# Kernel optimization log

Measured on AMD Instinct MI355X. Metric: run time of the kernel, lower is better.

Reference implementation:

```python
import jax, jax.numpy as jnp
import numpy as np

V = 100000   # vocab_size
E = 300      # embedding_dim
H = 512      # hidden_dim
HH = H // 2  # per-direction hidden
T = 24       # tagset size (incl START/STOP)
START, STOP = 22, 23
S = 4096     # sentence length
NEG = -10000.0


def setup_inputs() -> dict:
    key = jax.random.key(0)
    ks = jax.random.split(key, 12)
    sc = 0.05
    trans = jax.random.normal(ks[10], (T, T), jnp.float32) * 0.01
    # no transition INTO START, none OUT OF STOP (tutorial convention: trans[to, from])
    trans = trans.at[START, :].set(NEG).at[:, STOP].set(NEG)
    return {
        "sentence": jax.random.randint(ks[0], (S,), 0, V),
        "emb_table": jax.random.normal(ks[1], (V, E), jnp.float32) * sc,
        "w_ih_f": jax.random.normal(ks[2], (4 * HH, E), jnp.float32) * sc,
        "w_hh_f": jax.random.normal(ks[3], (4 * HH, HH), jnp.float32) * sc,
        "b_f": jnp.zeros((4 * HH,), jnp.float32),
        "w_ih_b": jax.random.normal(ks[4], (4 * HH, E), jnp.float32) * sc,
        "w_hh_b": jax.random.normal(ks[5], (4 * HH, HH), jnp.float32) * sc,
        "b_b": jnp.zeros((4 * HH,), jnp.float32),
        "w_tag": jax.random.normal(ks[6], (T, H), jnp.float32) * sc,
        "b_tag": jnp.zeros((T,), jnp.float32),
        "transitions": trans,
    }


def _lstm(x, w_ih, w_hh, b, reverse):
    # PyTorch LSTM gate order: i, f, g, o
    def step(carry, xt):
        h, c = carry
        g = xt @ w_ih.T + h @ w_hh.T + b
        i, f, gg, o = jnp.split(g, 4)
        c = jax.nn.sigmoid(f) * c + jax.nn.sigmoid(i) * jnp.tanh(gg)
        h = jax.nn.sigmoid(o) * jnp.tanh(c)
        return (h, c), h
    init = (jnp.zeros((HH,), x.dtype), jnp.zeros((HH,), x.dtype))
    _, hs = jax.lax.scan(step, init, x, reverse=reverse)
    return hs  # [S, HH], in original time order for both directions


def reference(sentence, emb_table, w_ih_f, w_hh_f, b_f, w_ih_b, w_hh_b, b_b,
              w_tag, b_tag, transitions):
    x = emb_table[sentence]                                   # [S, E]
    h = jnp.concatenate([_lstm(x, w_ih_f, w_hh_f, b_f, False),
                         _lstm(x, w_ih_b, w_hh_b, b_b, True)], axis=-1)  # [S, H]
    feats = h @ w_tag.T + b_tag                               # [S, T] emissions

    # Viterbi decode (tutorial _viterbi_decode)
    vinit = jnp.full((T,), NEG, feats.dtype).at[START].set(0.0)

    def vstep(v, feat):
        scores = v[None, :] + transitions                     # [to, from]
        return jnp.max(scores, axis=1) + feat, jnp.argmax(scores, axis=1)

    v, bptrs = jax.lax.scan(vstep, vinit, feats)              # bptrs: [S, T]
    term = v + transitions[STOP]
    best = jnp.argmax(term)
    score = term[best]

    def back(tag, bp):
        return bp[tag], tag

    _, path = jax.lax.scan(back, best, bptrs, reverse=True)   # [S] best tag seq
    return score, path
```

## Files before the change

kernel.cpp:

```cpp
#include <hip/hip_runtime.h>
#include <hip/hip_bf16.h>

#define S_LEN 4096
#define NTAG 24
#define START_TAG 22
#define STOP_TAG 23
#define SENT 0x7F800001u

static const size_t OFF_WT    = 0;
static const size_t OFF_XG    = OFF_WT + (size_t)300*2048*4;
static const size_t OFF_HS    = OFF_XG + (size_t)2*4096*1024*4;
static const size_t OFF_FEATS = OFF_HS + (size_t)2*4096*256*4;
static const size_t OFF_BP    = OFF_FEATS + (size_t)4096*24*4;
static const size_t OFF_WALK  = OFF_XG;

__device__ __forceinline__ float sigf(float x) {
    return __fdividef(1.f, 1.f + __expf(-x));
}
__device__ __forceinline__ float tanhfast(float x) {
    return 1.f - __fdividef(2.f, 1.f + __expf(2.f * x));
}

__device__ __forceinline__ float4 load_f4_sc1(const float* p) {
    float4 v;
    asm volatile("global_load_dwordx4 %0, %1, off sc1\n\t"
                 "s_waitcnt vmcnt(0)"
                 : "=v"(v) : "v"(p) : "memory");
    return v;
}

__device__ __forceinline__ float atomic_poll_word(const float* p) {
    float v;
    do {
        v = __hip_atomic_load(p, __ATOMIC_RELAXED, __HIP_MEMORY_SCOPE_AGENT);
    } while (__float_as_uint(v) == SENT);
    return v;
}

__global__ void prep_kernel(const float* __restrict__ w_ih_f, const float* __restrict__ w_ih_b,
                            float* __restrict__ WT, unsigned int* __restrict__ HSu) {
    int tid = blockIdx.x * blockDim.x + threadIdx.x;
    int nth = gridDim.x * blockDim.x;
    for (int idx = tid; idx < 300 * 2048; idx += nth) {
        int k = idx / 2048, col = idx % 2048;
        WT[idx] = (col < 1024) ? w_ih_f[col * 300 + k] : w_ih_b[(col - 1024) * 300 + k];
    }
    for (int idx = tid; idx < 2 * S_LEN * 256; idx += nth)
        HSu[idx] = SENT;
}

__global__ __launch_bounds__(256) void embed_xg_kernel(const int* __restrict__ sentence,
                                                       const float* __restrict__ emb,
                                                       const float* __restrict__ WT,
                                                       const float* __restrict__ b_f,
                                                       const float* __restrict__ b_b,
                                                       float* __restrict__ xg) {
    __shared__ float xs[16][300];
    int s0 = blockIdx.x * 16;
    for (int idx = threadIdx.x; idx < 16 * 300; idx += 256) {
        int si = idx / 300, k = idx - si * 300;
        int wrow = sentence[s0 + si];
        xs[si][k] = emb[(size_t)wrow * 300 + k];
    }
    __syncthreads();
    for (int chunk = 0; chunk < 8; ++chunk) {
        int col = chunk * 256 + threadIdx.x;
        float acc[16];
#pragma unroll
        for (int s = 0; s < 16; ++s) acc[s] = 0.f;
        for (int k = 0; k < 300; k += 4) {
            float w0 = WT[(k + 0) * 2048 + col];
            float w1 = WT[(k + 1) * 2048 + col];
            float w2 = WT[(k + 2) * 2048 + col];
            float w3 = WT[(k + 3) * 2048 + col];
#pragma unroll
            for (int s = 0; s < 16; ++s) {
                float4 x4 = *reinterpret_cast<const float4*>(&xs[s][k]);
                acc[s] += w0 * x4.x + w1 * x4.y + w2 * x4.z + w3 * x4.w;
            }
        }
        int dir = col >> 10;
        int row = col & 1023;
        float bias = dir ? b_b[row] : b_f[row];
#pragma unroll
        for (int s = 0; s < 16; ++s)
            xg[((size_t)dir * S_LEN + (s0 + s)) * 1024 + row] = acc[s] + bias;
    }
}

__global__ __launch_bounds__(1024) void lstm_kernel(const float* __restrict__ xg,
                                                    const float* __restrict__ w_hh_f,
                                                    const float* __restrict__ w_hh_b,
                                                    float* __restrict__ hs) {
    const int xslot = blockIdx.x & 7;
    if (xslot > 1) return;
    const int dir = xslot;
    const int blk = blockIdx.x >> 3;
    const int tid = threadIdx.x;
    const int r4 = tid >> 5;
    const int kc = tid & 31;

    __shared__ float hsk[32 * 10];
    __shared__ float part[128][33];
    __shared__ float gl[128];

    const float* whh = dir ? w_hh_b : w_hh_f;
    float w[4][8];
#pragma unroll
    for (int q = 0; q < 4; ++q) {
        int R = r4 * 4 + q;
        int grow = ((R >> 5) << 8) + blk * 32 + (R & 31);
#pragma unroll
        for (int j = 0; j < 8; ++j)
            w[q][j] = whh[(size_t)grow * 256 + kc * 8 + j];
    }

    for (int i = tid; i < 320; i += 1024) hsk[i] = 0.f;

    const float* xgd = xg + (size_t)dir * S_LEN * 1024;
    float* hsd = hs + (size_t)dir * S_LEN * 256;
    float c = 0.f;
    int growR = 0;
    float xg_cur = 0.f;
    if (tid < 128) {
        growR = ((tid >> 5) << 8) + blk * 32 + (tid & 31);
        xg_cur = xgd[(size_t)(dir ? (S_LEN - 1) : 0) * 1024 + growR];
    }
    __syncthreads();

    for (int step = 0; step < S_LEN; ++step) {
        const int st = dir ? (S_LEN - 1 - step) : step;

        float hv[8];
        const int hb = kc * 10;
#pragma unroll
        for (int j = 0; j < 8; ++j) hv[j] = hsk[hb + j];
        float p0 = 0.f, p1 = 0.f, p2 = 0.f, p3 = 0.f;
#pragma unroll
        for (int j = 0; j < 8; ++j) {
            p0 += w[0][j] * hv[j];
            p1 += w[1][j] * hv[j];
            p2 += w[2][j] * hv[j];
            p3 += w[3][j] * hv[j];
        }
        part[r4 * 4 + 0][kc] = p0;
        part[r4 * 4 + 1][kc] = p1;
        part[r4 * 4 + 2][kc] = p2;
        part[r4 * 4 + 3][kc] = p3;
        __syncthreads();

        float xg_nxt = 0.f;
        if (tid < 128) {
            if (step + 1 < S_LEN) {
                const int stn = dir ? (st - 1) : (st + 1);
                xg_nxt = xgd[(size_t)stn * 1024 + growR];
            }
            float a0 = 0.f, a1 = 0.f, a2 = 0.f, a3 = 0.f;
#pragma unroll
            for (int k2 = 0; k2 < 32; k2 += 4) {
                a0 += part[tid][k2 + 0];
                a1 += part[tid][k2 + 1];
                a2 += part[tid][k2 + 2];
                a3 += part[tid][k2 + 3];
            }
            gl[tid] = xg_cur + ((a0 + a1) + (a2 + a3));
        }
        __syncthreads();

        if (tid < 32) {
            float gi = gl[tid], gf = gl[32 + tid], gg = gl[64 + tid], go = gl[96 + tid];
            float si = sigf(gi), sf = sigf(gf), so = sigf(go);
            c = sf * c + si * tanhfast(gg);
            float h = so * tanhfast(c);
            __hip_atomic_store(&hsd[(size_t)st * 256 + blk * 32 + tid], h,
                               __ATOMIC_RELAXED, __HIP_MEMORY_SCOPE_AGENT);
            int w0 = blk * 32 + tid;
            hsk[(w0 >> 3) * 10 + (w0 & 7)] = h;
        }
        else if (tid >= 128 && tid < 192 && step + 1 < S_LEN) {
            const int l = tid - 128;
            if ((l >> 3) != blk) {
                const float* src = &hsd[(size_t)st * 256 + l * 4];
                float4 v;
                int spins = 0;
                bool ok;
                do {
                    v = load_f4_sc1(src);
                    ok = !(__float_as_uint(v.x) == SENT || __float_as_uint(v.y) == SENT ||
                           __float_as_uint(v.z) == SENT || __float_as_uint(v.w) == SENT);
                } while (!ok && ++spins < 512);
                if (!ok) {
                    v.x = atomic_poll_word(src + 0);
                    v.y = atomic_poll_word(src + 1);
                    v.z = atomic_poll_word(src + 2);
                    v.w = atomic_poll_word(src + 3);
                }
                const int w0 = l * 4;
                const int base = (w0 >> 3) * 10 + (w0 & 7);
                hsk[base + 0] = v.x;
                hsk[base + 1] = v.y;
                hsk[base + 2] = v.z;
                hsk[base + 3] = v.w;
            }
        }
        xg_cur = xg_nxt;
        __syncthreads();
    }
}

__global__ __launch_bounds__(384) void feats_kernel(const float* __restrict__ hs,
                                                    const float* __restrict__ w_tag,
                                                    const float* __restrict__ b_tag,
                                                    float* __restrict__ feats) {
    __shared__ float ht[16][512];
    int s0 = blockIdx.x * 16;
    for (int idx = threadIdx.x; idx < 16 * 512; idx += 384) {
        int si = idx >> 9, k = idx & 511;
        float v = (k < 256) ? hs[(size_t)(s0 + si) * 256 + k]
                            : hs[(size_t)S_LEN * 256 + (size_t)(s0 + si) * 256 + (k - 256)];
        ht[si][k] = v;
    }
    __syncthreads();
    int si = threadIdx.x / NTAG;
    int t = threadIdx.x - si * NTAG;
    float acc = b_tag[t];
    const float* wr = w_tag + t * 512;
    for (int k = 0; k < 512; k += 4) {
        float4 w4 = *reinterpret_cast<const float4*>(&wr[k]);
        float4 h4 = *reinterpret_cast<const float4*>(&ht[si][k]);
        acc += w4.x * h4.x + w4.y * h4.y + w4.z * h4.z + w4.w * h4.w;
    }
    feats[(size_t)(s0 + si) * NTAG + t] = acc;
}

__global__ __launch_bounds__(1024) void viterbi_kernel(const float* __restrict__ feats,
                                                       const float* __restrict__ trans,
                                                       unsigned char* __restrict__ bp_g,
                                                       unsigned char* __restrict__ walk_g,
                                                       float* __restrict__ out) {
    const int tid = threadIdx.x;
    __shared__ float s_bv;
    __shared__ int s_bti;
    __shared__ unsigned char maps[32][24];
    __shared__ int Bc[32];

    if (tid < 64) {
        const int lane = tid;
        const bool lo = lane < NTAG;
        const bool hi = (lane >= 32) && (lane < 32 + NTAG);
        const bool act = lo || hi;
        const int to = lo ? lane : lane - 32;
        const int fbase = lo ? 0 : 12;
        float wt[12];
#pragma unroll
        for (int j = 0; j < 12; ++j)
            wt[j] = act ? trans[to * NTAG + fbase + j] : -3.0e38f;
        float v = act ? ((to == START_TAG) ? 0.f : -10000.f) : -3.0e38f;
        float feat = act ? feats[to] : 0.f;

        for (int s = 0; s < S_LEN; ++s) {
            float featn = (act && s + 1 < S_LEN) ? feats[(s + 1) * NTAG + to] : 0.f;
            float m1 = -3.0e38f;
            int b1 = fbase;
#pragma unroll
            for (int j = 0; j < 12; ++j) {
                float cand = __shfl(v, fbase + j) + wt[j];
                if (cand > m1) { m1 = cand; b1 = fbase + j; }
            }
            float m2 = __shfl_xor(m1, 32);
            int b2 = __shfl_xor(b1, 32);
            float mlo = lo ? m1 : m2; int blo = lo ? b1 : b2;
            float mhi = lo ? m2 : m1; int bhi = lo ? b2 : b1;
            float m = fmaxf(mlo, mhi);
            int bi = (mhi > mlo) ? bhi : blo;
            v = m + feat;
            if (lo) bp_g[s * NTAG + lane] = (unsigned char)bi;
            feat = featn;
        }
        float wstop = act ? trans[STOP_TAG * NTAG + to] : 0.f;
        float bv = lo ? (v + wstop) : -3.0e38f;
        int bti = lo ? lane : 64;
#pragma unroll
        for (int d = 1; d < 64; d <<= 1) {
            float ov = __shfl_xor(bv, d);
            int oi = __shfl_xor(bti, d);
            if (ov > bv || (ov == bv && oi < bti)) { bv = ov; bti = oi; }
        }
        if (lane == 0) { s_bv = bv; s_bti = bti; }
    }
    __syncthreads();

    if (tid < 32 * NTAG) {
        const int c = tid / NTAG, E = tid - c * NTAG;
        const unsigned char* bpc = bp_g + (size_t)c * 128 * NTAG;
        unsigned char* wk = walk_g + (size_t)(c * NTAG + E) * 128;
        int m = E;
        wk[127] = (unsigned char)m;
        for (int j = 126; j >= 0; --j) {
            m = bpc[(j + 1) * NTAG + m];
            wk[j] = (unsigned char)m;
        }
        maps[c][E] = bpc[m];
    }
    __syncthreads();

    if (tid == 0) {
        int t = s_bti;
        for (int c = 31; c >= 0; --c) {
            Bc[c] = t;
            if (c) t = maps[c][t];
        }
        out[0] = s_bv;
    }
    __syncthreads();

    for (int i = tid; i < S_LEN; i += 1024) {
        int c = i >> 7, j = i & 127;
        out[1 + i] = (float)walk_g[(size_t)(c * NTAG + Bc[c]) * 128 + j];
    }
}

extern "C" void kernel_launch(void* const* d_in, const int* in_sizes, int n_in,
                              void* d_out, int out_size, void* d_ws, size_t ws_size,
                              hipStream_t stream) {
    const int*   sentence = (const int*)d_in[0];
    const float* emb      = (const float*)d_in[1];
    const float* w_ih_f   = (const float*)d_in[2];
    const float* w_hh_f   = (const float*)d_in[3];
    const float* b_f      = (const float*)d_in[4];
    const float* w_ih_b   = (const float*)d_in[5];
    const float* w_hh_b   = (const float*)d_in[6];
    const float* b_b      = (const float*)d_in[7];
    const float* w_tag    = (const float*)d_in[8];
    const float* b_tag    = (const float*)d_in[9];
    const float* trans    = (const float*)d_in[10];

    char* ws = (char*)d_ws;
    float*         WT    = (float*)(ws + OFF_WT);
    float*         XG    = (float*)(ws + OFF_XG);
    float*         HS    = (float*)(ws + OFF_HS);
    float*         FEATS = (float*)(ws + OFF_FEATS);
    unsigned char* BP    = (unsigned char*)(ws + OFF_BP);
    unsigned char* WALK  = (unsigned char*)(ws + OFF_WALK);

    float* out = (float*)d_out;

    prep_kernel<<<512, 256, 0, stream>>>(w_ih_f, w_ih_b, WT, (unsigned int*)HS);
    embed_xg_kernel<<<S_LEN / 16, 256, 0, stream>>>(sentence, emb, WT, b_f, b_b, XG);
    lstm_kernel<<<64, 1024, 0, stream>>>(XG, w_hh_f, w_hh_b, HS);
    feats_kernel<<<S_LEN / 16, 384, 0, stream>>>(HS, w_tag, b_tag, FEATS);
    viterbi_kernel<<<1, 1024, 0, stream>>>(FEATS, trans, BP, WALK, out);
}
```

Baseline: 8.276 ms.

## Poll peer hidden state per-word with atomics and move reducers to separate waves

Replaces the 64-thread float4 sc1 spin-load polling of other blocks' hidden-state slices with 256 threads (waves 4-7) that each atomically poll one word. The gate-reduction threads move from tid 0-127 to tid 512-639, so reducers and pollers sit in different wavefronts from the gate/cell threads. The goal is to cut cross-block handoff latency in the sequential LSTM recurrence and spread polling across more waves. The cost is more outstanding atomic polling traffic per step, plus 4x more scalar loads than the vectorized version.

```diff
diff --git a/kernel.cpp b/kernel.cpp
--- a/kernel.cpp
+++ b/kernel.cpp
@@ -19,14 +19,6 @@
 }
 __device__ __forceinline__ float tanhfast(float x) {
     return 1.f - __fdividef(2.f, 1.f + __expf(2.f * x));
-}
-
-__device__ __forceinline__ float4 load_f4_sc1(const float* p) {
-    float4 v;
-    asm volatile("global_load_dwordx4 %0, %1, off sc1\n\t"
-                 "s_waitcnt vmcnt(0)"
-                 : "=v"(v) : "v"(p) : "memory");
-    return v;
 }
 
 __device__ __forceinline__ float atomic_poll_word(const float* p) {
@@ -120,12 +112,17 @@
     const float* xgd = xg + (size_t)dir * S_LEN * 1024;
     float* hsd = hs + (size_t)dir * S_LEN * 256;
     float c = 0.f;
+
     int growR = 0;
     float xg_cur = 0.f;
-    if (tid < 128) {
-        growR = ((tid >> 5) << 8) + blk * 32 + (tid & 31);
+    const bool is_red = (tid >= 512 && tid < 640);
+    if (is_red) {
+        const int l = tid - 512;
+        growR = ((l >> 5) << 8) + blk * 32 + (l & 31);
         xg_cur = xgd[(size_t)(dir ? (S_LEN - 1) : 0) * 1024 + growR];
     }
+    const bool is_pol = (tid >= 256 && tid < 512) && (((tid - 256) >> 5) != blk);
+    const int pol_w = ((tid - 256) >> 5) * 32 + (tid & 31);
     __syncthreads();
 
     for (int step = 0; step < S_LEN; ++step) {
@@ -150,7 +147,8 @@
         __syncthreads();
 
         float xg_nxt = 0.f;
-        if (tid < 128) {
+        if (is_red) {
+            const int l = tid - 512;
             if (step + 1 < S_LEN) {
                 const int stn = dir ? (st - 1) : (st + 1);
                 xg_nxt = xgd[(size_t)stn * 1024 + growR];
@@ -158,12 +156,12 @@
             float a0 = 0.f, a1 = 0.f, a2 = 0.f, a3 = 0.f;
 #pragma unroll
             for (int k2 = 0; k2 < 32; k2 += 4) {
-                a0 += part[tid][k2 + 0];
-                a1 += part[tid][k2 + 1];
-                a2 += part[tid][k2 + 2];
-                a3 += part[tid][k2 + 3];
+                a0 += part[l][k2 + 0];
+                a1 += part[l][k2 + 1];
+                a2 += part[l][k2 + 2];
+                a3 += part[l][k2 + 3];
             }
-            gl[tid] = xg_cur + ((a0 + a1) + (a2 + a3));
+            gl[l] = xg_cur + ((a0 + a1) + (a2 + a3));
         }
         __syncthreads();
 
@@ -177,31 +175,9 @@
             int w0 = blk * 32 + tid;
             hsk[(w0 >> 3) * 10 + (w0 & 7)] = h;
         }
-        else if (tid >= 128 && tid < 192 && step + 1 < S_LEN) {
-            const int l = tid - 128;
-            if ((l >> 3) != blk) {
-                const float* src = &hsd[(size_t)st * 256 + l * 4];
-                float4 v;
-                int spins = 0;
-                bool ok;
-                do {
-                    v = load_f4_sc1(src);
-                    ok = !(__float_as_uint(v.x) == SENT || __float_as_uint(v.y) == SENT ||
-                           __float_as_uint(v.z) == SENT || __float_as_uint(v.w) == SENT);
-                } while (!ok && ++spins < 512);
-                if (!ok) {
-                    v.x = atomic_poll_word(src + 0);
-                    v.y = atomic_poll_word(src + 1);
-                    v.z = atomic_poll_word(src + 2);
-                    v.w = atomic_poll_word(src + 3);
-                }
-                const int w0 = l * 4;
-                const int base = (w0 >> 3) * 10 + (w0 & 7);
-                hsk[base + 0] = v.x;
-                hsk[base + 1] = v.y;
-                hsk[base + 2] = v.z;
-                hsk[base + 3] = v.w;
-            }
+        else if (is_pol && step + 1 < S_LEN) {
+            float v = atomic_poll_word(&hsd[(size_t)st * 256 + pol_w]);
+            hsk[(pol_w >> 3) * 10 + (pol_w & 7)] = v;
         }
         xg_cur = xg_nxt;
         __syncthreads();
```

Measured after the change: 8.770 ms. +6.0%, slower.
